# Performance work log

Hardware: AMD Instinct MI355X
Metric: run time of the kernel (lower is better)

## Reference

```python
import jax, jax.numpy as jnp
import numpy as np

HEAD_NUM = 8
NEG = 10000.0


def setup_inputs() -> dict:
    key = jax.random.key(0)
    ks = jax.random.split(key, 8)
    B, S, D = 2, 2048, 512
    sc = 1.0 / np.sqrt(D)
    return {
        "x": jax.random.normal(ks[0], (B, S, D), dtype=jnp.float32),
        "mask": jax.random.randint(ks[1], (B, S), 0, 2, dtype=jnp.int32),
        "Wq": jax.random.normal(ks[2], (D, D), dtype=jnp.float32) * sc,
        "bq": jnp.zeros((D,), jnp.float32),
        "Wk": jax.random.normal(ks[3], (D, D), dtype=jnp.float32) * sc,
        "bk": jnp.zeros((D,), jnp.float32),
        "Wv": jax.random.normal(ks[4], (D, D), dtype=jnp.float32) * sc,
        "bv": jnp.zeros((D,), jnp.float32),
        "Wo": jax.random.normal(ks[5], (D, D), dtype=jnp.float32) * sc,
        "bo": jnp.zeros((D,), jnp.float32),
    }


def _split_heads(t, H):
    B, S, D = t.shape
    return t.reshape(B, S, H, D // H).transpose(0, 2, 1, 3)  # [B,H,S,hd]


def reference(x, mask, Wq, bq, Wk, bk, Wv, bv, Wo, bo):
    B, S, D = x.shape
    H = HEAD_NUM
    hd = D // H
    # linear projections + relu activation (as in keras layer)
    q = jax.nn.relu(x @ Wq + bq)
    k = jax.nn.relu(x @ Wk + bk)
    v = jax.nn.relu(x @ Wv + bv)
    q = _split_heads(q, H)
    k = _split_heads(k, H)
    v = _split_heads(v, H)
    # scaled dot-product scores: scale by sqrt(head_dim) (query last dim after split)
    e = jnp.einsum("bhqd,bhkd->bhqk", q, k) / jnp.sqrt(jnp.float32(hd))
    # causal (history_only) additive mask
    idx = jnp.arange(S)
    causal = (idx[None, :] > idx[:, None]).astype(jnp.float32)  # [S,S]
    e = e - NEG * causal[None, None, :, :]
    # key padding mask, additive
    e = e - NEG * (1.0 - mask.astype(jnp.float32))[:, None, None, :]
    # stable softmax (explicit max-subtract as in source)
    a = jax.nn.softmax(e, axis=-1)
    out = jnp.einsum("bhqk,bhkd->bhqd", a, v)  # [B,H,S,hd]
    out = out.transpose(0, 2, 1, 3).reshape(B, S, D)
    # output projection + activation
    return jax.nn.relu(out @ Wo + bo)
```

## Files before the change

kernel.cpp:

```cpp
#include <hip/hip_runtime.h>
#include <hip/hip_bf16.h>

constexpr int Bc = 2, Sc = 2048, Dc = 512, Hc = 8, HDc = 64;
constexpr int Mtot = Bc * Sc;
constexpr size_t HEADMAT = (size_t)Bc * Hc * Sc * HDc;
constexpr float SC2  = 0.18033688011112042f;
constexpr float NEG2 = 14426.950408889634f;

typedef __attribute__((ext_vector_type(8)))  short          short8;
typedef __attribute__((ext_vector_type(8)))  unsigned short ushort8;
typedef __attribute__((ext_vector_type(4)))  float          f32x4;
typedef __attribute__((ext_vector_type(16))) float          f32x16;

#define MFMA16 __builtin_amdgcn_mfma_f32_16x16x32_bf16
#define MFMA32 __builtin_amdgcn_mfma_f32_32x32x16_bf16

static __device__ __forceinline__ unsigned short f32_to_bf16_bits(float f) {
    unsigned int u = __builtin_bit_cast(unsigned int, f);
    unsigned int r = u + 0x7FFFu + ((u >> 16) & 1u);
    return (unsigned short)(r >> 16);
}
static __device__ __forceinline__ unsigned int pkbf(float a, float b) {
    return (unsigned int)f32_to_bf16_bits(a) |
           ((unsigned int)f32_to_bf16_bits(b) << 16);
}

__global__ __launch_bounds__(256)
void convert_x(const float* __restrict__ x, unsigned short* __restrict__ Xb, int n)
{
    const int i = (blockIdx.x * 256 + threadIdx.x) * 4;
    if (i >= n) return;
    const float4 v = *(const float4*)(x + i);
    ushort4 o;
    o.x = f32_to_bf16_bits(v.x);
    o.y = f32_to_bf16_bits(v.y);
    o.z = f32_to_bf16_bits(v.z);
    o.w = f32_to_bf16_bits(v.w);
    *(ushort4*)(Xb + i) = o;
}

__global__ __launch_bounds__(256)
void transpose_w(const float* __restrict__ W0, const float* __restrict__ W1,
                 const float* __restrict__ W2, const float* __restrict__ W3,
                 unsigned short* __restrict__ Wt)
{
    __shared__ float T[64][65];
    const int z = blockIdx.z;
    const float* Wp = (z == 0) ? W0 : (z == 1) ? W1 : (z == 2) ? W2 : W3;
    unsigned short* Op = Wt + (size_t)z * 512 * 512;

    const int kt = blockIdx.y * 64, nt = blockIdx.x * 64;
    const int t = threadIdx.x;
    const int r  = t >> 2, c4 = (t & 3) * 16;

    #pragma unroll
    for (int i = 0; i < 4; ++i) {
        const float4 v = *(const float4*)(Wp + (size_t)(kt + r) * 512 + nt + c4 + 4 * i);
        T[r][c4 + 4*i + 0] = v.x;
        T[r][c4 + 4*i + 1] = v.y;
        T[r][c4 + 4*i + 2] = v.z;
        T[r][c4 + 4*i + 3] = v.w;
    }
    __syncthreads();

    const int n = t >> 2, k4 = (t & 3) * 16;
    #pragma unroll
    for (int i = 0; i < 4; ++i) {
        ushort4 o;
        o.x = f32_to_bf16_bits(T[k4 + 4*i + 0][n]);
        o.y = f32_to_bf16_bits(T[k4 + 4*i + 1][n]);
        o.z = f32_to_bf16_bits(T[k4 + 4*i + 2][n]);
        o.w = f32_to_bf16_bits(T[k4 + 4*i + 3][n]);
        *(ushort4*)(Op + (size_t)(nt + n) * 512 + kt + k4 + 4 * i) = o;
    }
}

template<bool HEADOUT>
__global__ __launch_bounds__(256)
void gemm_tile(const unsigned short* __restrict__ Xb,
               const unsigned short* __restrict__ Wt,
               const float* __restrict__ b0, const float* __restrict__ b1,
               const float* __restrict__ b2,
               unsigned short* __restrict__ Hout,
               float* __restrict__ Yf)
{
    __shared__ short As[128 * 32];
    __shared__ short Bs[64 * 32];

    const int lane = threadIdx.x & 63, wave = threadIdx.x >> 6;
    const int c = lane & 15, g = lane >> 4;
    const int wr = wave >> 1, wc = wave & 1;
    const int z = blockIdx.z;
    const unsigned short* Wp = Wt + (size_t)z * 512 * 512;
    const float* bp = (z == 0) ? b0 : (z == 1) ? b1 : b2;
    const int bm = blockIdx.y * 128;
    const int bn = blockIdx.x * 64;

    const int srow = lane >> 2;
    const int scol = (lane & 3) * 8;

    f32x4 acc[4][2] = {};

    for (int k0 = 0; k0 < 512; k0 += 32) {
        __syncthreads();
        #pragma unroll
        for (int i = 0; i < 2; ++i) {
            const int row = (wave * 2 + i) * 16 + srow;
            const short8 v = *(const short8*)(Xb + (size_t)(bm + row) * 512 + k0 + scol);
            *(short8*)(&As[row * 32 + scol]) = v;
        }
        {
            const int row = wave * 16 + srow;
            const short8 v = *(const short8*)(Wp + (size_t)(bn + row) * 512 + k0 + scol);
            *(short8*)(&Bs[row * 32 + scol]) = v;
        }
        __syncthreads();

        short8 a[4], bfr[2];
        #pragma unroll
        for (int mi = 0; mi < 4; ++mi)
            a[mi] = *(const short8*)(&As[(wr * 64 + mi * 16 + c) * 32 + g * 8]);
        #pragma unroll
        for (int ni = 0; ni < 2; ++ni)
            bfr[ni] = *(const short8*)(&Bs[(wc * 32 + ni * 16 + c) * 32 + g * 8]);
        #pragma unroll
        for (int mi = 0; mi < 4; ++mi)
            #pragma unroll
            for (int ni = 0; ni < 2; ++ni)
                acc[mi][ni] = MFMA16(a[mi], bfr[ni], acc[mi][ni], 0, 0, 0);
    }

    #pragma unroll
    for (int mi = 0; mi < 4; ++mi) {
        #pragma unroll
        for (int ni = 0; ni < 2; ++ni) {
            const int n = bn + wc * 32 + ni * 16 + c;
            const float bias = bp[n];
            float v[4];
            #pragma unroll
            for (int r = 0; r < 4; ++r)
                v[r] = fmaxf(acc[mi][ni][r] + bias, 0.0f);
            const int mbase = bm + wr * 64 + mi * 16 + 4 * g;
            if constexpr (HEADOUT) {
                const int bb = mbase >> 11, ss = mbase & 2047;
                const int hh = n >> 6, hd = n & 63;
                #pragma unroll
                for (int r = 0; r < 4; ++r)
                    Hout[(size_t)z * HEADMAT +
                         (((size_t)(bb * Hc + hh) * Sc + ss + r) * HDc + hd)] =
                        f32_to_bf16_bits(v[r]);
            } else {
                #pragma unroll
                for (int r = 0; r < 4; ++r)
                    Yf[(size_t)(mbase + r) * 512 + n] = v[r];
            }
        }
    }
}

__global__ __launch_bounds__(256)
void attn_mfma(const short* __restrict__ Qh, const short* __restrict__ Kh,
               const short* __restrict__ Vh, const int* __restrict__ mask,
               unsigned short* __restrict__ Ob)
{
    __shared__ __align__(16) char smem[4 * 8448 + 4 * 256];

    const int lane = threadIdx.x & 63;
    const int wave = threadIdx.x >> 6;
    const int bid  = blockIdx.x;
    const int swz  = (bid & 7) * 128 + (bid >> 3);
    const int t    = swz & 63;
    const int h    = (swz >> 6) & 7;
    const int b    = swz >> 9;
    const int q0   = t * 32;
    const int r32  = lane & 31;
    const int hi   = lane >> 5;

    char*  wreg = smem + wave * 8448;
    short* vst  = (short*)wreg;
    float* Lml  = (float*)(smem + 4 * 8448 + wave * 256);

    const size_t headoff = (size_t)(b * Hc + h) * Sc * HDc;
    const short* Qp = Qh + headoff;
    const short* Kp = Kh + headoff;
    const short* Vp = Vh + headoff;
    const int* mb = mask + b * Sc;

    int fb = Sc;
    for (int base = 0; base < Sc; base += 64) {
        unsigned long long bal = __ballot(mb[base + lane] != 0);
        if (bal) { fb = base + (__ffsll(bal) - 1); break; }
    }
    const int kmax = (fb <= q0) ? (q0 + 32) : Sc;
    const int kend = (kmax + 31) & ~31;
    const int nT   = kend >> 5;
    const int tpw  = (nT + 3) >> 2;
    const int kbeg = wave * tpw * 32;
    const int kfin = min(kend, kbeg + tpw * 32);

    short8 qf[4];
    #pragma unroll
    for (int j = 0; j < 4; ++j)
        qf[j] = *(const short8*)(Qp + (size_t)(q0 + r32) * HDc + j * 16 + hi * 8);

    f32x16 acc0 = {0,0,0,0,0,0,0,0,0,0,0,0,0,0,0,0};
    f32x16 acc1 = {0,0,0,0,0,0,0,0,0,0,0,0,0,0,0,0};
    float m = -1e30f, l = 0.0f;

    const int vrow = lane >> 1, vcol = (lane & 1) * 32;

    for (int k0 = kbeg; k0 < kfin; k0 += 32) {
        const short* vsrc = Vp + (size_t)(k0 + vrow) * HDc + vcol;
        const ushort8 vr0 = *(const ushort8*)(vsrc + 0);
        const ushort8 vr1 = *(const ushort8*)(vsrc + 8);
        const ushort8 vr2 = *(const ushort8*)(vsrc + 16);
        const ushort8 vr3 = *(const ushort8*)(vsrc + 24);

        f32x16 s = {0,0,0,0,0,0,0,0,0,0,0,0,0,0,0,0};
        #pragma unroll
        for (int j = 0; j < 4; ++j) {
            const short8 kf =
                *(const short8*)(Kp + (size_t)(k0 + r32) * HDc + j * 16 + hi * 8);
            s = MFMA32(kf, qf[j], s, 0, 0, 0);
        }

        const unsigned long long bal = __ballot(mb[k0 + r32] != 0);
        const unsigned int mloc = ((unsigned int)bal) >> (4 * hi);

        float e[16];
        float tmax = -1e30f;
        if (k0 + 31 > q0) {
            #pragma unroll
            for (int r = 0; r < 16; ++r) {
                const int cr0 = (r & 3) + 8 * (r >> 2);
                float ev = s[r] * SC2;
                if (!((mloc >> cr0) & 1))            ev -= NEG2;
                if (k0 + cr0 + 4 * hi > q0 + r32)    ev -= NEG2;
                e[r] = ev;
                tmax = fmaxf(tmax, ev);
            }
        } else {
            #pragma unroll
            for (int r = 0; r < 16; ++r) {
                const int cr0 = (r & 3) + 8 * (r >> 2);
                float ev = s[r] * SC2;
                if (!((mloc >> cr0) & 1))            ev -= NEG2;
                e[r] = ev;
                tmax = fmaxf(tmax, ev);
            }
        }
        tmax = fmaxf(tmax, __shfl_xor(tmax, 32));

        if (__any(tmax > m)) {
            const float mn   = fmaxf(m, tmax);
            const float corr = __builtin_exp2f(m - mn);
            m = mn; l *= corr;
            acc0 *= corr;
            acc1 *= corr;
        }

        float ps = 0.f;
        #pragma unroll
        for (int r = 0; r < 16; ++r) {
            e[r] = __builtin_exp2f(e[r] - m);
            ps += e[r];
        }
        l += ps;

        const unsigned int A0 = pkbf(e[0],  e[1]),  B0 = pkbf(e[2],  e[3]);
        const unsigned int C0 = pkbf(e[4],  e[5]),  D0 = pkbf(e[6],  e[7]);
        const unsigned int A1 = pkbf(e[8],  e[9]),  B1 = pkbf(e[10], e[11]);
        const unsigned int C1 = pkbf(e[12], e[13]), D1 = pkbf(e[14], e[15]);
        const unsigned int A0s = (unsigned int)__shfl_xor((int)A0, 32);
        const unsigned int B0s = (unsigned int)__shfl_xor((int)B0, 32);
        const unsigned int C0s = (unsigned int)__shfl_xor((int)C0, 32);
        const unsigned int D0s = (unsigned int)__shfl_xor((int)D0, 32);
        const unsigned int A1s = (unsigned int)__shfl_xor((int)A1, 32);
        const unsigned int B1s = (unsigned int)__shfl_xor((int)B1, 32);
        const unsigned int C1s = (unsigned int)__shfl_xor((int)C1, 32);
        const unsigned int D1s = (unsigned int)__shfl_xor((int)D1, 32);

        union { unsigned int u[4]; short8 s8; } P0, P1;
        P0.u[0] = hi ? C0s : A0;  P0.u[1] = hi ? D0s : B0;
        P0.u[2] = hi ? C0  : A0s; P0.u[3] = hi ? D0  : B0s;
        P1.u[0] = hi ? C1s : A1;  P1.u[1] = hi ? D1s : B1;
        P1.u[2] = hi ? C1  : A1s; P1.u[3] = hi ? D1  : B1s;

        short* vdst = vst + vrow * 72 + vcol;
        *(ushort8*)(vdst + 0)  = vr0;
        *(ushort8*)(vdst + 8)  = vr1;
        *(ushort8*)(vdst + 16) = vr2;
        *(ushort8*)(vdst + 24) = vr3;

        short8 va;
        #pragma unroll
        for (int e8 = 0; e8 < 8; ++e8)
            va[e8] = vst[(8 * hi + e8) * 72 + r32];
        acc0 = MFMA32(va, P0.s8, acc0, 0, 0, 0);
        #pragma unroll
        for (int e8 = 0; e8 < 8; ++e8)
            va[e8] = vst[(16 + 8 * hi + e8) * 72 + r32];
        acc0 = MFMA32(va, P1.s8, acc0, 0, 0, 0);
        #pragma unroll
        for (int e8 = 0; e8 < 8; ++e8)
            va[e8] = vst[(8 * hi + e8) * 72 + 32 + r32];
        acc1 = MFMA32(va, P0.s8, acc1, 0, 0, 0);
        #pragma unroll
        for (int e8 = 0; e8 < 8; ++e8)
            va[e8] = vst[(16 + 8 * hi + e8) * 72 + 32 + r32];
        acc1 = MFMA32(va, P1.s8, acc1, 0, 0, 0);
    }

    l += __shfl_xor(l, 32);

    {
        float* Lacc = (float*)wreg;
        #pragma unroll
        for (int r = 0; r < 16; ++r) {
            Lacc[lane * 33 + r]      = acc0[r];
            Lacc[lane * 33 + 16 + r] = acc1[r];
        }
        if (lane < 32) { Lml[lane] = m; Lml[32 + lane] = l; }
    }
    __syncthreads();

    float mu[4], lu[4], M = -1e30f;
    #pragma unroll
    for (int u = 0; u < 4; ++u) {
        const float* LmlU = (const float*)(smem + 4 * 8448 + u * 256);
        mu[u] = LmlU[r32];
        lu[u] = LmlU[32 + r32];
        M = fmaxf(M, mu[u]);
    }
    float wgt[4], L = 0.f;
    #pragma unroll
    for (int u = 0; u < 4; ++u) {
        wgt[u] = __builtin_exp2f(mu[u] - M);
        L += wgt[u] * lu[u];
    }
    const float invL = 1.0f / L;

    #pragma unroll
    for (int jj = 0; jj < 8; ++jj) {
        const int j = wave * 8 + jj;
        float o = 0.f;
        #pragma unroll
        for (int u = 0; u < 4; ++u)
            o += wgt[u] * ((const float*)(smem + u * 8448))[lane * 33 + j];
        const int j16 = j & 15;
        const int d = (j16 & 3) + 8 * (j16 >> 2) + 4 * hi + 32 * (j >> 4);
        Ob[(size_t)(b * Sc + q0 + r32) * Dc + h * HDc + d] =
            f32_to_bf16_bits(o * invL);
    }
}

extern "C" void kernel_launch(void* const* d_in, const int* in_sizes, int n_in,
                              void* d_out, int out_size, void* d_ws, size_t ws_size,
                              hipStream_t stream) {
    const float* x  = (const float*)d_in[0];
    const int* mask = (const int*)d_in[1];
    const float* Wq = (const float*)d_in[2];
    const float* bq = (const float*)d_in[3];
    const float* Wk = (const float*)d_in[4];
    const float* bk = (const float*)d_in[5];
    const float* Wv = (const float*)d_in[6];
    const float* bv = (const float*)d_in[7];
    const float* Wo = (const float*)d_in[8];
    const float* bo = (const float*)d_in[9];
    float* out = (float*)d_out;

    unsigned short* Xb = (unsigned short*)d_ws;
    unsigned short* Wt = Xb + (size_t)Mtot * 512;
    unsigned short* Qh = Wt + (size_t)4 * 512 * 512;
    unsigned short* Kh = Qh + HEADMAT;
    unsigned short* Vh = Kh + HEADMAT;
    unsigned short* Ob = Vh + HEADMAT;

    convert_x<<<dim3((Mtot * 512) / 1024), dim3(256), 0, stream>>>(
        x, Xb, Mtot * 512);
    transpose_w<<<dim3(8, 8, 4), dim3(256), 0, stream>>>(Wq, Wk, Wv, Wo, Wt);
    gemm_tile<true><<<dim3(8, Mtot / 128, 3), dim3(256), 0, stream>>>(
        Xb, Wt, bq, bk, bv, Qh, nullptr);
    attn_mfma<<<dim3(1024), dim3(256), 0, stream>>>(
        (const short*)Qh, (const short*)Kh, (const short*)Vh, mask, Ob);
    gemm_tile<false><<<dim3(8, Mtot / 128, 1), dim3(256), 0, stream>>>(
        Ob, Wt + (size_t)3 * 512 * 512, bo, bo, bo, nullptr, out);
}
```

Measured before the change: 95.98 us.

## Store V transposed from projection GEMM and load MFMA operands directly

The QKV projection now writes V in a transposed [b,h,hd,S] layout using packed 4-element stores. The attention kernel then loads the V operand fragments for the PV MFMAs straight from global memory. This drops the per-iteration LDS staging round trip and the strided scalar LDS gathers. In exchange, the V reads become row-strided across Sc, which may hurt coalescing or cache behaviour.

```diff
diff --git a/kernel.cpp b/kernel.cpp
--- a/kernel.cpp
+++ b/kernel.cpp
@@ -144,11 +144,20 @@
             if constexpr (HEADOUT) {
                 const int bb = mbase >> 11, ss = mbase & 2047;
                 const int hh = n >> 6, hd = n & 63;
-                #pragma unroll
-                for (int r = 0; r < 4; ++r)
-                    Hout[(size_t)z * HEADMAT +
-                         (((size_t)(bb * Hc + hh) * Sc + ss + r) * HDc + hd)] =
-                        f32_to_bf16_bits(v[r]);
+                if (z == 2) {
+                    union { ushort4 u; unsigned short s[4]; } pk;
+                    #pragma unroll
+                    for (int r = 0; r < 4; ++r) pk.s[r] = f32_to_bf16_bits(v[r]);
+                    *reinterpret_cast<ushort4*>(
+                        Hout + (size_t)2 * HEADMAT +
+                        ((size_t)(bb * Hc + hh) * HDc + hd) * Sc + ss) = pk.u;
+                } else {
+                    #pragma unroll
+                    for (int r = 0; r < 4; ++r)
+                        Hout[(size_t)z * HEADMAT +
+                             (((size_t)(bb * Hc + hh) * Sc + ss + r) * HDc + hd)] =
+                            f32_to_bf16_bits(v[r]);
+                }
             } else {
                 #pragma unroll
                 for (int r = 0; r < 4; ++r)
@@ -160,7 +169,7 @@
 
 __global__ __launch_bounds__(256)
 void attn_mfma(const short* __restrict__ Qh, const short* __restrict__ Kh,
-               const short* __restrict__ Vh, const int* __restrict__ mask,
+               const short* __restrict__ Vt, const int* __restrict__ mask,
                unsigned short* __restrict__ Ob)
 {
     __shared__ __align__(16) char smem[4 * 8448 + 4 * 256];
@@ -177,13 +186,12 @@
     const int hi   = lane >> 5;
 
     char*  wreg = smem + wave * 8448;
-    short* vst  = (short*)wreg;
     float* Lml  = (float*)(smem + 4 * 8448 + wave * 256);
 
     const size_t headoff = (size_t)(b * Hc + h) * Sc * HDc;
     const short* Qp = Qh + headoff;
     const short* Kp = Kh + headoff;
-    const short* Vp = Vh + headoff;
+    const short* Vp = Vt + headoff;
     const int* mb = mask + b * Sc;
 
     int fb = Sc;
@@ -207,14 +215,14 @@
     f32x16 acc1 = {0,0,0,0,0,0,0,0,0,0,0,0,0,0,0,0};
     float m = -1e30f, l = 0.0f;
 
-    const int vrow = lane >> 1, vcol = (lane & 1) * 32;
+    const short* vrow0 = Vp + (size_t)r32 * Sc + 8 * hi;
+    const short* vrow1 = Vp + (size_t)(32 + r32) * Sc + 8 * hi;
 
     for (int k0 = kbeg; k0 < kfin; k0 += 32) {
-        const short* vsrc = Vp + (size_t)(k0 + vrow) * HDc + vcol;
-        const ushort8 vr0 = *(const ushort8*)(vsrc + 0);
-        const ushort8 vr1 = *(const ushort8*)(vsrc + 8);
-        const ushort8 vr2 = *(const ushort8*)(vsrc + 16);
-        const ushort8 vr3 = *(const ushort8*)(vsrc + 24);
+        const short8 va0 = *(const short8*)(vrow0 + k0);
+        const short8 va1 = *(const short8*)(vrow0 + k0 + 16);
+        const short8 vb0 = *(const short8*)(vrow1 + k0);
+        const short8 vb1 = *(const short8*)(vrow1 + k0 + 16);
 
         f32x16 s = {0,0,0,0,0,0,0,0,0,0,0,0,0,0,0,0};
         #pragma unroll
@@ -286,29 +294,10 @@
         P1.u[0] = hi ? C1s : A1;  P1.u[1] = hi ? D1s : B1;
         P1.u[2] = hi ? C1  : A1s; P1.u[3] = hi ? D1  : B1s;
 
-        short* vdst = vst + vrow * 72 + vcol;
-        *(ushort8*)(vdst + 0)  = vr0;
-        *(ushort8*)(vdst + 8)  = vr1;
-        *(ushort8*)(vdst + 16) = vr2;
-        *(ushort8*)(vdst + 24) = vr3;
-
-        short8 va;
-        #pragma unroll
-        for (int e8 = 0; e8 < 8; ++e8)
-            va[e8] = vst[(8 * hi + e8) * 72 + r32];
-        acc0 = MFMA32(va, P0.s8, acc0, 0, 0, 0);
-        #pragma unroll
-        for (int e8 = 0; e8 < 8; ++e8)
-            va[e8] = vst[(16 + 8 * hi + e8) * 72 + r32];
-        acc0 = MFMA32(va, P1.s8, acc0, 0, 0, 0);
-        #pragma unroll
-        for (int e8 = 0; e8 < 8; ++e8)
-            va[e8] = vst[(8 * hi + e8) * 72 + 32 + r32];
-        acc1 = MFMA32(va, P0.s8, acc1, 0, 0, 0);
-        #pragma unroll
-        for (int e8 = 0; e8 < 8; ++e8)
-            va[e8] = vst[(16 + 8 * hi + e8) * 72 + 32 + r32];
-        acc1 = MFMA32(va, P1.s8, acc1, 0, 0, 0);
+        acc0 = MFMA32(va0, P0.s8, acc0, 0, 0, 0);
+        acc0 = MFMA32(va1, P1.s8, acc0, 0, 0, 0);
+        acc1 = MFMA32(vb0, P0.s8, acc1, 0, 0, 0);
+        acc1 = MFMA32(vb1, P1.s8, acc1, 0, 0, 0);
     }
 
     l += __shfl_xor(l, 32);
@@ -373,8 +362,8 @@
     unsigned short* Wt = Xb + (size_t)Mtot * 512;
     unsigned short* Qh = Wt + (size_t)4 * 512 * 512;
     unsigned short* Kh = Qh + HEADMAT;
-    unsigned short* Vh = Kh + HEADMAT;
-    unsigned short* Ob = Vh + HEADMAT;
+    unsigned short* Vt = Kh + HEADMAT;
+    unsigned short* Ob = Vt + HEADMAT;
 
     convert_x<<<dim3((Mtot * 512) / 1024), dim3(256), 0, stream>>>(
         x, Xb, Mtot * 512);
@@ -382,7 +371,7 @@
     gemm_tile<true><<<dim3(8, Mtot / 128, 3), dim3(256), 0, stream>>>(
         Xb, Wt, bq, bk, bv, Qh, nullptr);
     attn_mfma<<<dim3(1024), dim3(256), 0, stream>>>(
-        (const short*)Qh, (const short*)Kh, (const short*)Vh, mask, Ob);
+        (const short*)Qh, (const short*)Kh, (const short*)Vt, mask, Ob);
     gemm_tile<false><<<dim3(8, Mtot / 128, 1), dim3(256), 0, stream>>>(
         Ob, Wt + (size_t)3 * 512 * 512, bo, bo, bo, nullptr, out);
 }
```

Result: no change. 97.49 us (+1.6%).
